# Optimization experiments

Measured on AMD Instinct MI355X. Metric: run time of the kernel, lower is better.

Reference implementation:

```python
import jax, jax.numpy as jnp
import numpy as np
from functools import partial

CONF_THRESH = 0.01
NMS_THRESH = 0.45
TOP_K = 200


def setup_inputs() -> dict:
    key = jax.random.key(0)
    k1, k2, k3 = jax.random.split(key, 3)
    B, N, C = 256, 8732, 21
    loc_data = jax.random.normal(k1, (B, N, 4), dtype=jnp.float32)
    conf_data = jax.random.normal(k2, (B, N, C), dtype=jnp.float32)
    dbox_list = jax.random.uniform(k3, (N, 4), dtype=jnp.float32)
    return {"loc_data": loc_data, "conf_data": conf_data, "dbox_list": dbox_list}


def decode(loc, dbox):
    # loc, dbox: (N, 4). Faithful to torch decode: variances 0.1 / 0.2.
    cxcy = dbox[:, :2] + loc[:, :2] * 0.1 * dbox[:, 2:]
    wh = dbox[:, 2:] * jnp.exp(loc[:, 2:] * 0.2)
    xymin = cxcy - wh / 2.0
    xymax = xymin + wh
    return jnp.concatenate([xymin, xymax], axis=1)  # (N,4) xmin,ymin,xmax,ymax


def nms_single(boxes, scores):
    # boxes: (N,4), scores: (N,). Returns (TOP_K, 5) rows [conf, x1, y1, x2, y2]
    # compacted to the front in descending-score keep order (matches torch output[i,cl,:count]).
    masked = jnp.where(scores > CONF_THRESH, scores, -1.0)
    top_scores, top_idx = jax.lax.top_k(masked, TOP_K)
    b = boxes[top_idx]  # (TOP_K, 4)
    x1, y1, x2, y2 = b[:, 0], b[:, 1], b[:, 2], b[:, 3]
    area = (x2 - x1) * (y2 - y1)
    valid = top_scores > CONF_THRESH

    def body(i, state):
        suppressed, keep = state
        active = jnp.logical_not(suppressed[i])
        keep = keep.at[i].set(active)
        # Faithful to source: all four coords are clamped with min=coord[i]
        # (i.e. elementwise max), including x2/y2 -- reproducing the original math.
        xx1 = jnp.maximum(x1, x1[i])
        yy1 = jnp.maximum(y1, y1[i])
        xx2 = jnp.maximum(x2, x2[i])
        yy2 = jnp.maximum(y2, y2[i])
        inter = (xx2 - xx1) * (yy2 - yy1)
        union = area - inter + area[i]
        iou = inter / union
        sup_new = jnp.logical_and(active, iou > NMS_THRESH)
        sup_new = sup_new.at[i].set(False)
        return jnp.logical_or(suppressed, sup_new), keep

    suppressed0 = jnp.logical_not(valid)
    keep0 = jnp.zeros((TOP_K,), dtype=bool)
    suppressed, keep = jax.lax.fori_loop(0, TOP_K, body, (suppressed0, keep0))

    rows = jnp.concatenate([top_scores[:, None], b], axis=1)  # (TOP_K, 5)
    rows = jnp.where(keep[:, None], rows, 0.0)
    dest = jnp.where(keep, jnp.cumsum(keep) - 1, TOP_K)  # dump slot TOP_K
    out = jnp.zeros((TOP_K + 1, 5), dtype=boxes.dtype).at[dest].set(rows)
    return out[:TOP_K]


def reference(loc_data, conf_data, dbox_list):
    # loc_data: (B, 8732, 4); conf_data: (B, 8732, 21); dbox_list: (8732, 4)
    conf = jax.nn.softmax(conf_data, axis=-1)          # (B, N, C)
    conf_preds = jnp.transpose(conf, (0, 2, 1))        # (B, C, N)
    decoded = jax.vmap(decode, in_axes=(0, None))(loc_data, dbox_list)  # (B, N, 4)
    per_class = jax.vmap(lambda bx, sc: jax.vmap(lambda s: nms_single(bx, s))(sc))(
        decoded, conf_preds
    )  # (B, C, TOP_K, 5)
    # class 0 is background and is skipped in the torch loop -> zeros
    return per_class.at[:, 0].set(0.0)
```

## Files before the change

### kernel.cpp

```cpp
#include <hip/hip_runtime.h>
#include <cstdint>

#pragma clang fp contract(off)

#define TPB 256
typedef unsigned int uint32;
typedef unsigned short u16;
typedef unsigned long long u64;

constexpr int BB = 256;
constexpr int NN = 8732;
constexpr int CC = 21;
constexpr int KK = 200;
constexpr int CH = (NN + TPB - 1) / TPB;
constexpr uint32 KBIAS = 0x3C23D70Au;

__device__ __forceinline__ double fexp(double a) {
  const double L2E = 1.4426950408889634074;
  const double SHIFT = 6755399441055744.0;
  double t = __builtin_fma(a, L2E, SHIFT);
  int i = (int)__double_as_longlong(t);
  double n = t - SHIFT;
  double r = __builtin_fma(n, -6.93147180369123816490e-01, a);
  r = __builtin_fma(n, -1.90821492927058770002e-10, r);
  double p = 1.6059043836821614599e-10;
  p = __builtin_fma(p, r, 2.0876756987868098979e-9);
  p = __builtin_fma(p, r, 2.5052108385441718775e-8);
  p = __builtin_fma(p, r, 2.7557319223985890653e-7);
  p = __builtin_fma(p, r, 2.7557319223985890653e-6);
  p = __builtin_fma(p, r, 2.4801587301587301587e-5);
  p = __builtin_fma(p, r, 1.9841269841269841270e-4);
  p = __builtin_fma(p, r, 1.3888888888888888889e-3);
  p = __builtin_fma(p, r, 8.3333333333333333333e-3);
  p = __builtin_fma(p, r, 4.1666666666666666667e-2);
  p = __builtin_fma(p, r, 1.6666666666666666667e-1);
  p = __builtin_fma(p, r, 0.5);
  p = __builtin_fma(p, r, 1.0);
  p = __builtin_fma(p, r, 1.0);
  return p * __longlong_as_double((long long)(1023 + i) << 52);
}

__device__ __forceinline__ float exp_f32_exact(float xf) {
  double v = fexp((double)xf);
  uint32 low29 = (uint32)__double_as_longlong(v) & 0x1FFFFFFFu;
  uint32 dist = (low29 > 0x10000000u) ? (low29 - 0x10000000u) : (0x10000000u - low29);
  if (__builtin_expect(dist <= 65536u, 0)) v = exp((double)xf);
  return (float)v;
}

__device__ __forceinline__ u64 rfl64(u64 v) {
  uint32 lo = (uint32)__builtin_amdgcn_readfirstlane((int)(uint32)v);
  uint32 hi = (uint32)__builtin_amdgcn_readfirstlane((int)(uint32)(v >> 32));
  return ((u64)hi << 32) | lo;
}

struct NmsS {
  alignas(16) float bx1[256];
  alignas(16) float by1[256];
  alignas(16) float bx2[256];
  alignas(16) float by2[256];
  alignas(16) float barea[256];
  alignas(16) float bscore[256];
  alignas(16) u64 mask[KK][4];
  u64 kept[4];
};
struct SmemT {
  union alignas(16) UU {
    u16 s16[NN];
    NmsS nms;
  } u;
  union alignas(16) HC {
    uint32 hist[512];
    u64 cand[256];
  } hc;
  uint32 sc4[4];
  uint32 bc[3];
  uint32 slot;
};
static_assert(sizeof(SmemT) <= 20 * 1024, "LDS budget for 8 blocks/CU");

__device__ __forceinline__ uint32 kk_of(float p) {
  return (p > 0.01f) ? (__float_as_uint(p) - KBIAS) : 0u;
}

__device__ __forceinline__ void scan_find(SmemT& sm, uint32 target, int t, int lane, int wv,
                                          uint32& pivot, uint32& cntabove, uint32& pivcnt,
                                          uint32& total) {
  uint32 h0 = sm.hc.hist[2 * t], h1 = sm.hc.hist[2 * t + 1];
  uint32 part = h0 + h1;
  uint32 suf = part;
  for (int off = 1; off < 64; off <<= 1) {
    uint32 v = __shfl_down(suf, off, 64);
    if (lane + off < 64) suf += v;
  }
  if (lane == 0) sm.sc4[wv] = suf;
  __syncthreads();
  uint32 tot = sm.sc4[0] + sm.sc4[1] + sm.sc4[2] + sm.sc4[3];
  uint32 add = 0;
  for (int w = wv + 1; w < 4; ++w) add += sm.sc4[w];
  uint32 mine = suf + add, nxt = mine - part;
  if (mine >= target && nxt < target) {
    uint32 acc = nxt + h1;
    if (acc >= target) { sm.bc[0] = 2u * t + 1u; sm.bc[1] = nxt; sm.bc[2] = h1; }
    else               { sm.bc[0] = 2u * t;      sm.bc[1] = acc; sm.bc[2] = h0; }
  }
  __syncthreads();
  sm.hc.hist[2 * t] = 0u;
  sm.hc.hist[2 * t + 1] = 0u;
  pivot = sm.bc[0];
  cntabove = sm.bc[1];
  pivcnt = sm.bc[2];
  total = tot;
  __syncthreads();
}

template <int MODE>
__global__ __launch_bounds__(TPB, 5) void prep_kernel(const float* __restrict__ conf,
                                                      float* __restrict__ probsT,
                                                      double2* __restrict__ ms) {
  __shared__ float tile[TPB * CC];
  const int blk = blockIdx.x;
  const int b = blockIdx.y;
  const int n0 = blk * TPB;
  const int cnt = (NN - n0 < TPB) ? (NN - n0) : TPB;
  const size_t base = ((size_t)b * NN + n0) * CC;
  if (cnt == TPB) {
    const float4* s4 = (const float4*)(conf + base);
    float4* t4 = (float4*)tile;
    for (int i = threadIdx.x; i < (TPB * CC) / 4; i += TPB) t4[i] = s4[i];
  } else {
    for (int i = threadIdx.x; i < cnt * CC; i += TPB) tile[i] = conf[base + i];
  }
  __syncthreads();
  if (threadIdx.x >= cnt) return;
  const int n = n0 + threadIdx.x;
  const float* cp = tile + threadIdx.x * CC;
  float mx = cp[0];
#pragma unroll
  for (int j = 1; j < CC; ++j) mx = fmaxf(mx, cp[j]);
  const double mxd = (double)mx;

  if (MODE == 0) {
    double es1[CC - 1];
    double S = fexp((double)cp[0] - mxd);
#pragma unroll
    for (int j = 1; j < CC; ++j) {
      es1[j - 1] = fexp((double)cp[j] - mxd);
      S += es1[j - 1];
    }
    const double Sinv = 1.0 / S;
    bool slow = false;
    float* op = probsT + (size_t)b * 20 * NN + n;
#pragma unroll
    for (int c2 = 1; c2 < CC; ++c2) {
      double ph = es1[c2 - 1] * Sinv;
      uint32 low29 = (uint32)__double_as_longlong(ph) & 0x1FFFFFFFu;
      uint32 dist = (low29 > 0x10000000u) ? (low29 - 0x10000000u) : (0x10000000u - low29);
      slow = slow || (dist <= 320u) || (ph < 1e-30);
      op[(size_t)(c2 - 1) * NN] = (float)ph;
    }
    if (__builtin_expect(slow, 0)) {
      double es2[CC];
      double S2 = 0.0;
      for (int j = 0; j < CC; ++j) {
        es2[j] = exp((double)cp[j] - mxd);
        S2 += es2[j];
      }
      double Si2 = 1.0 / S2;
      for (int c2 = 1; c2 < CC; ++c2) op[(size_t)(c2 - 1) * NN] = (float)(es2[c2] * Si2);
    }
  } else {
    double S = 0.0;
#pragma unroll
    for (int j = 0; j < CC; ++j) S += exp((double)cp[j] - mxd);
    ms[(size_t)b * NN + n] = make_double2(mxd, 1.0 / S);
  }
}

template <int MODE>
__device__ __forceinline__ float prob_one(const float* __restrict__ prow,
                                          const float* __restrict__ conf,
                                          const double2* __restrict__ ms,
                                          int b, int c, int n) {
  if (MODE == 0) {
    return prow[n];
  } else if (MODE == 1) {
    double2 mv = ms[(size_t)b * NN + n];
    float x = conf[((size_t)b * NN + n) * CC + c];
    return (float)(exp((double)x - mv.x) * mv.y);
  } else {
    const float* cp = conf + ((size_t)b * NN + n) * CC;
    float mx = cp[0];
    for (int j = 1; j < CC; ++j) mx = fmaxf(mx, cp[j]);
    double S = 0.0, ec = 0.0;
    for (int j = 0; j < CC; ++j) {
      double e = exp((double)cp[j] - (double)mx);
      S += e;
      if (j == c) ec = e;
    }
    return (float)(ec * (1.0 / S));
  }
}

__device__ __forceinline__ bool iou_gt(float inter, float uni) {
  const float MDf = 0x1.CCCCCDp-2f;
  float pq = MDf * uni;
  float er = __builtin_fmaf(MDf, uni, -pq);
  return (inter > pq) | ((inter == pq) & (er < 0.0f));
}

__device__ __forceinline__ void mask_unit32(NmsS& nm, int r, int c) {
  const float xi1 = nm.bx1[r], yi1 = nm.by1[r];
  const float xi2 = nm.bx2[r], yi2 = nm.by2[r];
  const float ai = nm.barea[r];
  const int jbeg = c * 32;
  uint32 w = 0;
#pragma unroll
  for (int j0 = jbeg; j0 < jbeg + 32; j0 += 4) {
    const float4 q1 = *(const float4*)&nm.bx1[j0];
    const float4 q2 = *(const float4*)&nm.by1[j0];
    const float4 q3 = *(const float4*)&nm.bx2[j0];
    const float4 q4 = *(const float4*)&nm.by2[j0];
    const float4 qa = *(const float4*)&nm.barea[j0];
    const float a1[4] = {q1.x, q1.y, q1.z, q1.w};
    const float a2[4] = {q2.x, q2.y, q2.z, q2.w};
    const float a3[4] = {q3.x, q3.y, q3.z, q3.w};
    const float a4[4] = {q4.x, q4.y, q4.z, q4.w};
    const float aa[4] = {qa.x, qa.y, qa.z, qa.w};
#pragma unroll
    for (int e = 0; e < 4; ++e) {
      const int j = j0 + e;
      float xx1 = fmaxf(a1[e], xi1);
      float yy1 = fmaxf(a2[e], yi1);
      float xx2 = fmaxf(a3[e], xi2);
      float yy2 = fmaxf(a4[e], yi2);
      float inter = (xx2 - xx1) * (yy2 - yy1);
      float uni = (aa[e] - inter) + ai;
      bool sup = (uni >= 0.0f) && iou_gt(inter, uni);
      if (sup) w |= 1u << (j & 31);
    }
  }
  const int d = r - jbeg;
  if (d >= 0) w &= (0xFFFFFFFEu << d);
  ((uint32*)&nm.mask[r][0])[c] = w;
}

__device__ __forceinline__ void mask_unit_short(NmsS& nm, int r) {
  const float xi1 = nm.bx1[r], yi1 = nm.by1[r];
  const float xi2 = nm.bx2[r], yi2 = nm.by2[r];
  const float ai = nm.barea[r];
  uint32 w = 0;
#pragma unroll
  for (int j0 = 192; j0 < 200; j0 += 4) {
    const float4 q1 = *(const float4*)&nm.bx1[j0];
    const float4 q2 = *(const float4*)&nm.by1[j0];
    const float4 q3 = *(const float4*)&nm.bx2[j0];
    const float4 q4 = *(const float4*)&nm.by2[j0];
    const float4 qa = *(const float4*)&nm.barea[j0];
    const float a1[4] = {q1.x, q1.y, q1.z, q1.w};
    const float a2[4] = {q2.x, q2.y, q2.z, q2.w};
    const float a3[4] = {q3.x, q3.y, q3.z, q3.w};
    const float a4[4] = {q4.x, q4.y, q4.z, q4.w};
    const float aa[4] = {qa.x, qa.y, qa.z, qa.w};
#pragma unroll
    for (int e = 0; e < 4; ++e) {
      const int j = j0 + e;
      float xx1 = fmaxf(a1[e], xi1);
      float yy1 = fmaxf(a2[e], yi1);
      float xx2 = fmaxf(a3[e], xi2);
      float yy2 = fmaxf(a4[e], yi2);
      float inter = (xx2 - xx1) * (yy2 - yy1);
      float uni = (aa[e] - inter) + ai;
      bool sup = (uni >= 0.0f) && iou_gt(inter, uni);
      if (sup) w |= 1u << (j & 31);
    }
  }
  const int d = r - 192;
  if (d >= 0) w &= (0xFFFFFFFEu << d);
  ((uint32*)&nm.mask[r][0])[6] = w;
}

template <int MODE>
__global__ __launch_bounds__(TPB, 8) void nms_kernel(
    const float* __restrict__ probsT, const float* __restrict__ conf,
    const double2* __restrict__ ms, const float* __restrict__ loc,
    const float* __restrict__ dbox, float* __restrict__ out) {
  __shared__ SmemT sm;
  const int t = threadIdx.x;
  const int lane = t & 63;
  const int wv = t >> 6;
  const int tb = blockIdx.x;
  const int xcd = tb & 7;
  const int s0i = tb >> 3;
  const int bi = s0i / CC;
  const int c = s0i - bi * CC;
  const int b = bi * 8 + xcd;
  const size_t outbase = (size_t)(b * CC + c) * KK * 5;

  if (c == 0) {
    for (int i = t; i < KK * 5; i += TPB) out[outbase + i] = 0.0f;
    return;
  }
  const float* prow = (MODE == 0) ? probsT + ((size_t)b * 20 + (c - 1)) * NN : nullptr;

  sm.hc.hist[t] = 0u;
  sm.hc.hist[t + 256] = 0u;
  if (t == 0) sm.slot = 0u;
  __syncthreads();

  if (MODE == 0) {
    const float4* p4 = (const float4*)prow;
    for (int i = t; i < NN / 4; i += TPB) {
      float4 p = p4[i];
      uint32 k0 = kk_of(p.x), k1 = kk_of(p.y), k2 = kk_of(p.z), k3 = kk_of(p.w);
      uint32 s0 = k0 ? (k0 >> 10) + 1u : 0u;
      uint32 s1 = k1 ? (k1 >> 10) + 1u : 0u;
      uint32 s2 = k2 ? (k2 >> 10) + 1u : 0u;
      uint32 s3 = k3 ? (k3 >> 10) + 1u : 0u;
      ((u64*)sm.u.s16)[i] = (u64)s0 | ((u64)s1 << 16) | ((u64)s2 << 32) | ((u64)s3 << 48);
      if (s0) atomicAdd(&sm.hc.hist[s0 >> 8], 1u);
      if (s1) atomicAdd(&sm.hc.hist[s1 >> 8], 1u);
      if (s2) atomicAdd(&sm.hc.hist[s2 >> 8], 1u);
      if (s3) atomicAdd(&sm.hc.hist[s3 >> 8], 1u);
    }
  } else {
    for (int n = t; n < NN; n += TPB) {
      uint32 k = kk_of(prob_one<MODE>(prow, conf, ms, b, c, n));
      uint32 s = k ? (k >> 10) + 1u : 0u;
      sm.u.s16[n] = (u16)s;
      if (s) atomicAdd(&sm.hc.hist[s >> 8], 1u);
    }
  }
  __syncthreads();
  uint32 P0, cg0, pc0, total;
  scan_find(sm, (uint32)KK, t, lane, wv, P0, cg0, pc0, total);

  const bool few = total < (uint32)KK;
  uint32 P16, cgA = 0, eqc = 0, ncand;
  if (!few) {
    for (int i = t; i < NN / 2; i += TPB) {
      uint32 w = ((const uint32*)sm.u.s16)[i];
      uint32 a = w & 0xFFFFu, bq = w >> 16;
      if ((a >> 8) == P0) atomicAdd(&sm.hc.hist[a & 0xFFu], 1u);
      if ((bq >> 8) == P0) atomicAdd(&sm.hc.hist[bq & 0xFFu], 1u);
    }
    __syncthreads();
    uint32 P1, cg1, pc1, tot1;
    scan_find(sm, (uint32)KK - cg0, t, lane, wv, P1, cg1, pc1, tot1);
    P16 = (P0 << 8) | P1;
    cgA = cg0 + cg1;
    eqc = pc1;
    ncand = cgA + eqc;
  } else {
    P16 = 1u;
    ncand = total;
  }

  u64 val = 0;
  if (ncand <= 256u) {
    sm.hc.cand[t] = 0ull;
    __syncthreads();
    for (int i = t; i < NN / 2; i += TPB) {
      uint32 w = ((const uint32*)sm.u.s16)[i];
      uint32 a = w & 0xFFFFu, bq = w >> 16;
      if (a >= P16) { uint32 s = atomicAdd(&sm.slot, 1u); sm.hc.cand[s] = (u64)(2 * i); }
      if (bq >= P16) { uint32 s = atomicAdd(&sm.slot, 1u); sm.hc.cand[s] = (u64)(2 * i + 1); }
    }
    __syncthreads();
    if (few) {
      const int base = t * CH;
      const int endn = (base + CH < NN) ? (base + CH) : NN;
      uint32 cz = 0;
      for (int n = base; n < endn; ++n) cz += (sm.u.s16[n] == 0);
      uint32 incl = cz;
      for (int off = 1; off < 64; off <<= 1) {
        uint32 v = __shfl_up(incl, off, 64);
        if (lane >= off) incl += v;
      }
      if (lane == 63) sm.sc4[wv] = incl;
      __syncthreads();
      uint32 add = 0;
      for (int w2 = 0; w2 < wv; ++w2) add += sm.sc4[w2];
      uint32 g = add + incl - cz;
      const uint32 npad = (uint32)KK - ncand;
      if (cz && g < npad) {
        for (int n = base; n < endn && g < npad; ++n)
          if (sm.u.s16[n] == 0) { sm.hc.cand[ncand + g] = (u64)n; ++g; }
      }
      __syncthreads();
    }
    const uint32 ntot = few ? (uint32)KK : ncand;
    if (t < (int)ntot) {
      uint32 idx = (uint32)sm.hc.cand[t];
      uint32 k = (t < (int)ncand) ? kk_of(prob_one<MODE>(prow, conf, ms, b, c, (int)idx)) : 0u;
      val = ((u64)k << 32) | (uint32)(~idx);
    }
  } else {
    const uint32 BK = P16 - 1u;
    const uint32 tgt = (uint32)KK - cgA;
    for (int n = t; n < NN; n += TPB) {
      uint32 k = kk_of(prob_one<MODE>(prow, conf, ms, b, c, n));
      if (k && (k >> 10) == BK) atomicAdd(&sm.hc.hist[(k >> 5) & 31u], 1u);
    }
    __syncthreads();
    uint32 q0, d0, px, tx;
    scan_find(sm, tgt, t, lane, wv, q0, d0, px, tx);
    for (int n = t; n < NN; n += TPB) {
      uint32 k = kk_of(prob_one<MODE>(prow, conf, ms, b, c, n));
      if (k && (k >> 5) == ((BK << 5) | q0)) atomicAdd(&sm.hc.hist[k & 31u], 1u);
    }
    __syncthreads();
    uint32 q1, d1, py, ty;
    scan_find(sm, tgt - d0, t, lane, wv, q1, d1, py, ty);
    const uint32 T = (BK << 10) | (q0 << 5) | q1;
    const uint32 cnt_gt = cgA + d0 + d1;
    const uint32 m_need = (uint32)KK - cnt_gt;
    sm.hc.cand[t] = 0ull;
    if (t == 0) sm.slot = 0u;
    __syncthreads();
    const int base = t * CH;
    const int endn = (base + CH < NN) ? (base + CH) : NN;
    uint32 cnteq = 0;
    for (int n = base; n < endn; ++n) {
      uint32 k = kk_of(prob_one<MODE>(prow, conf, ms, b, c, n));
      if (k > T) {
        uint32 s = atomicAdd(&sm.slot, 1u);
        sm.hc.cand[s] = ((u64)k << 32) | (uint32)(~(uint32)n);
      }
      cnteq += (k == T);
    }
    uint32 incl = cnteq;
    for (int off = 1; off < 64; off <<= 1) {
      uint32 v = __shfl_up(incl, off, 64);
      if (lane >= off) incl += v;
    }
    if (lane == 63) sm.sc4[wv] = incl;
    __syncthreads();
    uint32 add = 0;
    for (int w2 = 0; w2 < wv; ++w2) add += sm.sc4[w2];
    uint32 g = add + incl - cnteq;
    if (cnteq && g < m_need) {
      for (int n = base; n < endn && g < m_need; ++n) {
        uint32 k = kk_of(prob_one<MODE>(prow, conf, ms, b, c, n));
        if (k == T) {
          sm.hc.cand[cnt_gt + g] = ((u64)T << 32) | (uint32)(~(uint32)n);
          ++g;
        }
      }
    }
    __syncthreads();
    val = sm.hc.cand[t];
  }

  for (int kk = 2; kk <= 256; kk <<= 1) {
    for (int j = kk >> 1; j > 0; j >>= 1) {
      u64 other;
      if (j >= 64) {
        __syncthreads();
        sm.hc.cand[t] = val;
        __syncthreads();
        other = sm.hc.cand[t ^ j];
      } else {
        other = __shfl_xor((unsigned long long)val, j, 64);
      }
      const bool takeMax = ((t & kk) == 0) == ((t & j) == 0);
      val = takeMax ? (val > other ? val : other) : (val < other ? val : other);
    }
  }
  __syncthreads();

  if (t < KK) {
    uint32 k32 = (uint32)(val >> 32);
    uint32 idx = ~((uint32)val);
    bool valid = k32 != 0u;
    float score = valid ? __uint_as_float(k32 + KBIAS) : -1.0f;
    const float4 lc = ((const float4*)loc)[(size_t)b * NN + idx];
    const float4 db = ((const float4*)dbox)[idx];
    float cx = db.x + (lc.x * 0.1f) * db.z;
    float cy = db.y + (lc.y * 0.1f) * db.w;
    float w_ = db.z * exp_f32_exact(lc.z * 0.2f);
    float h_ = db.w * exp_f32_exact(lc.w * 0.2f);
    float x1 = cx - w_ * 0.5f;
    float y1 = cy - h_ * 0.5f;
    float x2 = x1 + w_;
    float y2 = y1 + h_;
    sm.u.nms.bx1[t] = x1;
    sm.u.nms.by1[t] = y1;
    sm.u.nms.bx2[t] = x2;
    sm.u.nms.by2[t] = y2;
    sm.u.nms.barea[t] = (x2 - x1) * (y2 - y1);
    sm.u.nms.bscore[t] = score;
  } else {
    sm.u.nms.bscore[t] = -1.0f;
  }
  __syncthreads();

  {
    {
      int u = t;
      int cq = (u >= 192) ? ((u >= 480) ? 5 : ((u >= 320) ? 4 : 3))
                          : ((u >= 96) ? 2 : ((u >= 32) ? 1 : 0));
      int off = 16 * cq * (cq + 1);
      mask_unit32(sm.u.nms, u - off, cq);
    }
    {
      int u = 256 + t;
      int cq = (u >= 480) ? 5 : ((u >= 320) ? 4 : 3);
      int off = 16 * cq * (cq + 1);
      mask_unit32(sm.u.nms, u - off, cq);
    }
    if (t < 160) {
      int u = 512 + t;
      mask_unit32(sm.u.nms, u - 480, 5);
    }
    if (t < KK) mask_unit_short(sm.u.nms, t);
  }
  __syncthreads();

  if (wv == 0) {
    u64 s0 = __ballot(!(sm.u.nms.bscore[lane] > 0.01f));
    u64 s1 = __ballot(!(sm.u.nms.bscore[64 + lane] > 0.01f));
    u64 s2 = __ballot(!(sm.u.nms.bscore[128 + lane] > 0.01f));
    u64 s3 = __ballot(!(sm.u.nms.bscore[192 + lane] > 0.01f)) | ~0xFFull;
    u64 k0 = 0, k1 = 0, k2 = 0, k3 = 0;
    const u64(*M)[4] = sm.u.nms.mask;
    u64 pre[4][4];
#pragma unroll
    for (int s = 0; s < 4; ++s) {
      ulonglong2 a = ((const ulonglong2*)M[s])[0];
      ulonglong2 bb = ((const ulonglong2*)M[s])[1];
      pre[s][0] = a.x; pre[s][1] = a.y; pre[s][2] = bb.x; pre[s][3] = bb.y;
    }
#define WALK_BLOCK(SW, KW, CNT, IBASE)                                   \
  _Pragma("unroll 4")                                                    \
  for (int ii = 0; ii < (CNT); ++ii) {                                   \
    const int s = ii & 3;                                                \
    u64 bm = 1ull << ii;                                                 \
    if (!((SW) & bm)) {                                                  \
      (KW) |= bm;                                                        \
      s0 |= rfl64(pre[s][0]); s1 |= rfl64(pre[s][1]);                    \
      s2 |= rfl64(pre[s][2]); s3 |= rfl64(pre[s][3]);                    \
    }                                                                    \
    const int inext = (IBASE) + ii + 4;                                  \
    ulonglong2 na = ((const ulonglong2*)M[inext])[0];                    \
    ulonglong2 nb = ((const ulonglong2*)M[inext])[1];                    \
    pre[s][0] = na.x; pre[s][1] = na.y; pre[s][2] = nb.x; pre[s][3] = nb.y; \
  }
    WALK_BLOCK(s0, k0, 64, 0)
    WALK_BLOCK(s1, k1, 64, 64)
    WALK_BLOCK(s2, k2, 64, 128)
    WALK_BLOCK(s3, k3, 8, 192)
#undef WALK_BLOCK
    if (lane == 0) {
      sm.u.nms.kept[0] = k0; sm.u.nms.kept[1] = k1;
      sm.u.nms.kept[2] = k2; sm.u.nms.kept[3] = k3;
    }
  } else {
    float4 z4 = make_float4(0.f, 0.f, 0.f, 0.f);
    float4* o4 = (float4*)(out + outbase);
    for (int i = t - 64; i < (KK * 5) / 4; i += 192) o4[i] = z4;
  }
  __syncthreads();

  if (t < KK) {
    const u64 K0 = sm.u.nms.kept[0], K1 = sm.u.nms.kept[1];
    const u64 K2 = sm.u.nms.kept[2], K3 = sm.u.nms.kept[3];
    const int w = t >> 6;
    const int bit = t & 63;
    u64 kw = (w == 0) ? K0 : (w == 1) ? K1 : (w == 2) ? K2 : K3;
    bool kp = (kw >> bit) & 1ull;
    if (kp) {
      u64 lowm = (bit == 0) ? 0ull : (~0ull >> (64 - bit));
      int d = __popcll(kw & lowm);
      if (w > 0) d += __popcll(K0);
      if (w > 1) d += __popcll(K1);
      if (w > 2) d += __popcll(K2);
      float* o = out + outbase + (size_t)d * 5;
      o[0] = sm.u.nms.bscore[t];
      o[1] = sm.u.nms.bx1[t];
      o[2] = sm.u.nms.by1[t];
      o[3] = sm.u.nms.bx2[t];
      o[4] = sm.u.nms.by2[t];
    }
  }
}

extern "C" void kernel_launch(void* const* d_in, const int* in_sizes, int n_in,
                              void* d_out, int out_size, void* d_ws, size_t ws_size,
                              hipStream_t stream) {
  (void)in_sizes; (void)n_in; (void)out_size;
  const float* loc = (const float*)d_in[0];
  const float* conf = (const float*)d_in[1];
  const float* dbox = (const float*)d_in[2];
  float* out = (float*)d_out;

  const size_t needA = (size_t)BB * 20 * NN * sizeof(float);
  const size_t needB = (size_t)BB * NN * sizeof(double2);
  dim3 blk(TPB);
  dim3 g1((NN + TPB - 1) / TPB, BB);
  const int g2 = BB * CC;

  if (ws_size >= needA) {
    float* probsT = (float*)d_ws;
    prep_kernel<0><<<g1, blk, 0, stream>>>(conf, probsT, nullptr);
    nms_kernel<0><<<g2, blk, 0, stream>>>(probsT, conf, nullptr, loc, dbox, out);
  } else if (ws_size >= needB) {
    double2* msp = (double2*)d_ws;
    prep_kernel<1><<<g1, blk, 0, stream>>>(conf, nullptr, msp);
    nms_kernel<1><<<g2, blk, 0, stream>>>(nullptr, conf, msp, loc, dbox, out);
  } else {
    nms_kernel<2><<<g2, blk, 0, stream>>>(nullptr, conf, nullptr, loc, dbox, out);
  }
}
```

Measured before the change: 439.5 us.

## Store 16-bit coarse keys instead of float probabilities in workspace

The prep kernel now writes only the 16-bit coarse histogram key for each class probability, plus a per-anchor (max, 1/sum) pair, instead of a full float probability array. The NMS kernel reads the keys directly for the first histogram pass. Exact probabilities are recomputed on demand from conf plus the stored max and reciprocal sum, with a flag for the slow exact-exp path. This halves the intermediate write and read traffic, at the cost of recomputation in the refinement and candidate passes and an extra ms array.

```diff
diff --git a/kernel.cpp b/kernel.cpp
--- a/kernel.cpp
+++ b/kernel.cpp
@@ -116,7 +116,7 @@
 
 template <int MODE>
 __global__ __launch_bounds__(TPB, 5) void prep_kernel(const float* __restrict__ conf,
-                                                      float* __restrict__ probsT,
+                                                      u16* __restrict__ keys,
                                                       double2* __restrict__ ms) {
   __shared__ float tile[TPB * CC];
   const int blk = blockIdx.x;
@@ -150,15 +150,17 @@
     }
     const double Sinv = 1.0 / S;
     bool slow = false;
-    float* op = probsT + (size_t)b * 20 * NN + n;
+    u16* kp = keys + (size_t)b * 20 * NN + n;
 #pragma unroll
     for (int c2 = 1; c2 < CC; ++c2) {
       double ph = es1[c2 - 1] * Sinv;
       uint32 low29 = (uint32)__double_as_longlong(ph) & 0x1FFFFFFFu;
       uint32 dist = (low29 > 0x10000000u) ? (low29 - 0x10000000u) : (0x10000000u - low29);
       slow = slow || (dist <= 320u) || (ph < 1e-30);
-      op[(size_t)(c2 - 1) * NN] = (float)ph;
-    }
+      uint32 k = kk_of((float)ph);
+      kp[(size_t)(c2 - 1) * NN] = (u16)(k ? (k >> 10) + 1u : 0u);
+    }
+    double Sy = Sinv;
     if (__builtin_expect(slow, 0)) {
       double es2[CC];
       double S2 = 0.0;
@@ -167,8 +169,13 @@
         S2 += es2[j];
       }
       double Si2 = 1.0 / S2;
-      for (int c2 = 1; c2 < CC; ++c2) op[(size_t)(c2 - 1) * NN] = (float)(es2[c2] * Si2);
-    }
+      for (int c2 = 1; c2 < CC; ++c2) {
+        uint32 k = kk_of((float)(es2[c2] * Si2));
+        kp[(size_t)(c2 - 1) * NN] = (u16)(k ? (k >> 10) + 1u : 0u);
+      }
+      Sy = -Si2;
+    }
+    ms[(size_t)b * NN + n] = make_double2(mxd, Sy);
   } else {
     double S = 0.0;
 #pragma unroll
@@ -178,12 +185,24 @@
 }
 
 template <int MODE>
-__device__ __forceinline__ float prob_one(const float* __restrict__ prow,
-                                          const float* __restrict__ conf,
+__device__ __forceinline__ float prob_sel(const float* __restrict__ conf,
                                           const double2* __restrict__ ms,
                                           int b, int c, int n) {
   if (MODE == 0) {
-    return prow[n];
+    double2 mv = ms[(size_t)b * NN + n];
+    if (__builtin_expect(mv.y < 0.0, 0)) {
+      const float* cp = conf + ((size_t)b * NN + n) * CC;
+      double S2 = 0.0, ec = 0.0;
+      for (int j = 0; j < CC; ++j) {
+        double e = exp((double)cp[j] - mv.x);
+        S2 += e;
+        if (j == c) ec = e;
+      }
+      double Si2 = 1.0 / S2;
+      return (float)(ec * Si2);
+    }
+    float x = conf[((size_t)b * NN + n) * CC + c];
+    return (float)(fexp((double)x - mv.x) * mv.y);
   } else if (MODE == 1) {
     double2 mv = ms[(size_t)b * NN + n];
     float x = conf[((size_t)b * NN + n) * CC + c];
@@ -282,7 +301,7 @@
 
 template <int MODE>
 __global__ __launch_bounds__(TPB, 8) void nms_kernel(
-    const float* __restrict__ probsT, const float* __restrict__ conf,
+    const u16* __restrict__ keys, const float* __restrict__ conf,
     const double2* __restrict__ ms, const float* __restrict__ loc,
     const float* __restrict__ dbox, float* __restrict__ out) {
   __shared__ SmemT sm;
@@ -301,7 +320,6 @@
     for (int i = t; i < KK * 5; i += TPB) out[outbase + i] = 0.0f;
     return;
   }
-  const float* prow = (MODE == 0) ? probsT + ((size_t)b * 20 + (c - 1)) * NN : nullptr;
 
   sm.hc.hist[t] = 0u;
   sm.hc.hist[t + 256] = 0u;
@@ -309,15 +327,14 @@
   __syncthreads();
 
   if (MODE == 0) {
-    const float4* p4 = (const float4*)prow;
+    const u16* krow = keys + ((size_t)b * 20 + (c - 1)) * NN;
+    const u64* k4 = (const u64*)krow;
     for (int i = t; i < NN / 4; i += TPB) {
-      float4 p = p4[i];
-      uint32 k0 = kk_of(p.x), k1 = kk_of(p.y), k2 = kk_of(p.z), k3 = kk_of(p.w);
-      uint32 s0 = k0 ? (k0 >> 10) + 1u : 0u;
-      uint32 s1 = k1 ? (k1 >> 10) + 1u : 0u;
-      uint32 s2 = k2 ? (k2 >> 10) + 1u : 0u;
-      uint32 s3 = k3 ? (k3 >> 10) + 1u : 0u;
-      ((u64*)sm.u.s16)[i] = (u64)s0 | ((u64)s1 << 16) | ((u64)s2 << 32) | ((u64)s3 << 48);
+      u64 w4 = k4[i];
+      ((u64*)sm.u.s16)[i] = w4;
+      uint32 lo = (uint32)w4, hi = (uint32)(w4 >> 32);
+      uint32 s0 = lo & 0xFFFFu, s1 = lo >> 16;
+      uint32 s2 = hi & 0xFFFFu, s3 = hi >> 16;
       if (s0) atomicAdd(&sm.hc.hist[s0 >> 8], 1u);
       if (s1) atomicAdd(&sm.hc.hist[s1 >> 8], 1u);
       if (s2) atomicAdd(&sm.hc.hist[s2 >> 8], 1u);
@@ -325,7 +342,7 @@
     }
   } else {
     for (int n = t; n < NN; n += TPB) {
-      uint32 k = kk_of(prob_one<MODE>(prow, conf, ms, b, c, n));
+      uint32 k = kk_of(prob_sel<MODE>(conf, ms, b, c, n));
       uint32 s = k ? (k >> 10) + 1u : 0u;
       sm.u.s16[n] = (u16)s;
       if (s) atomicAdd(&sm.hc.hist[s >> 8], 1u);
@@ -392,21 +409,21 @@
     const uint32 ntot = few ? (uint32)KK : ncand;
     if (t < (int)ntot) {
       uint32 idx = (uint32)sm.hc.cand[t];
-      uint32 k = (t < (int)ncand) ? kk_of(prob_one<MODE>(prow, conf, ms, b, c, (int)idx)) : 0u;
+      uint32 k = (t < (int)ncand) ? kk_of(prob_sel<MODE>(conf, ms, b, c, (int)idx)) : 0u;
       val = ((u64)k << 32) | (uint32)(~idx);
     }
   } else {
     const uint32 BK = P16 - 1u;
     const uint32 tgt = (uint32)KK - cgA;
     for (int n = t; n < NN; n += TPB) {
-      uint32 k = kk_of(prob_one<MODE>(prow, conf, ms, b, c, n));
+      uint32 k = kk_of(prob_sel<MODE>(conf, ms, b, c, n));
       if (k && (k >> 10) == BK) atomicAdd(&sm.hc.hist[(k >> 5) & 31u], 1u);
     }
     __syncthreads();
     uint32 q0, d0, px, tx;
     scan_find(sm, tgt, t, lane, wv, q0, d0, px, tx);
     for (int n = t; n < NN; n += TPB) {
-      uint32 k = kk_of(prob_one<MODE>(prow, conf, ms, b, c, n));
+      uint32 k = kk_of(prob_sel<MODE>(conf, ms, b, c, n));
       if (k && (k >> 5) == ((BK << 5) | q0)) atomicAdd(&sm.hc.hist[k & 31u], 1u);
     }
     __syncthreads();
@@ -422,7 +439,7 @@
     const int endn = (base + CH < NN) ? (base + CH) : NN;
     uint32 cnteq = 0;
     for (int n = base; n < endn; ++n) {
-      uint32 k = kk_of(prob_one<MODE>(prow, conf, ms, b, c, n));
+      uint32 k = kk_of(prob_sel<MODE>(conf, ms, b, c, n));
       if (k > T) {
         uint32 s = atomicAdd(&sm.slot, 1u);
         sm.hc.cand[s] = ((u64)k << 32) | (uint32)(~(uint32)n);
@@ -441,7 +458,7 @@
     uint32 g = add + incl - cnteq;
     if (cnteq && g < m_need) {
       for (int n = base; n < endn && g < m_need; ++n) {
-        uint32 k = kk_of(prob_one<MODE>(prow, conf, ms, b, c, n));
+        uint32 k = kk_of(prob_sel<MODE>(conf, ms, b, c, n));
         if (k == T) {
           sm.hc.cand[cnt_gt + g] = ((u64)T << 32) | (uint32)(~(uint32)n);
           ++g;
@@ -594,16 +611,19 @@
   const float* dbox = (const float*)d_in[2];
   float* out = (float*)d_out;
 
-  const size_t needA = (size_t)BB * 20 * NN * sizeof(float);
-  const size_t needB = (size_t)BB * NN * sizeof(double2);
+  const size_t keysBytes = (size_t)BB * 20 * NN * sizeof(u16);
+  const size_t msBytes = (size_t)BB * NN * sizeof(double2);
+  const size_t needA = keysBytes + msBytes;
+  const size_t needB = msBytes;
   dim3 blk(TPB);
   dim3 g1((NN + TPB - 1) / TPB, BB);
   const int g2 = BB * CC;
 
   if (ws_size >= needA) {
-    float* probsT = (float*)d_ws;
-    prep_kernel<0><<<g1, blk, 0, stream>>>(conf, probsT, nullptr);
-    nms_kernel<0><<<g2, blk, 0, stream>>>(probsT, conf, nullptr, loc, dbox, out);
+    u16* keys = (u16*)d_ws;
+    double2* msp = (double2*)((char*)d_ws + keysBytes);
+    prep_kernel<0><<<g1, blk, 0, stream>>>(conf, keys, msp);
+    nms_kernel<0><<<g2, blk, 0, stream>>>(keys, conf, msp, loc, dbox, out);
   } else if (ws_size >= needB) {
     double2* msp = (double2*)d_ws;
     prep_kernel<1><<<g1, blk, 0, stream>>>(conf, nullptr, msp);
```

Result: no change. 439.1 us (-0.1%).
